# Performance work log

Measured on AMD Instinct MI355X. Metric: run time of the kernel, lower is better.

The kernel has to match this reference:

```python
import jax, jax.numpy as jnp
import numpy as np

N_HEADS = 32
ROPE_THETA = 10000.0


def _rope_cos_sin(sl, head_dim, dtype):
    # inv_freq over even dims, HF/Llama convention: emb = concat(freqs, freqs)
    inv_freq = 1.0 / (ROPE_THETA ** (jnp.arange(0, head_dim, 2, dtype=jnp.float32) / head_dim))
    pos = jnp.arange(sl, dtype=jnp.float32)
    freqs = pos[:, None] * inv_freq[None, :]            # [sl, hd/2]
    emb = jnp.concatenate([freqs, freqs], axis=-1)       # [sl, hd]
    return jnp.cos(emb).astype(dtype), jnp.sin(emb).astype(dtype)


def _rotate_half(x):
    h = x.shape[-1] // 2
    return jnp.concatenate([-x[..., h:], x[..., :h]], axis=-1)


def setup_inputs() -> dict:
    key = jax.random.key(0)
    ks = jax.random.split(key, 5)
    bs, sl, hs = 2, 2048, 4096
    scale = hs ** -0.5
    return {
        "hidden_states": jax.random.normal(ks[0], (bs, sl, hs), jnp.float32),
        "wq": jax.random.normal(ks[1], (hs, hs), jnp.float32) * scale,
        "wk": jax.random.normal(ks[2], (hs, hs), jnp.float32) * scale,
        "wv": jax.random.normal(ks[3], (hs, hs), jnp.float32) * scale,
        "wo": jax.random.normal(ks[4], (hs, hs), jnp.float32) * scale,
    }


def reference(hidden_states, wq, wk, wv, wo):
    bs, sl, hs = hidden_states.shape
    hd = hs // N_HEADS
    # QKV projections (nn.Linear without bias: x @ W.T; here W stored as [in,out])
    q = hidden_states @ wq
    k = hidden_states @ wk
    v = hidden_states @ wv
    # [bs, sl, H, hd]
    q = q.reshape(bs, sl, N_HEADS, hd)
    k = k.reshape(bs, sl, N_HEADS, hd)
    v = v.reshape(bs, sl, N_HEADS, hd)
    # Vectorized RoPE across the whole sequence (original loops per position)
    cos, sin = _rope_cos_sin(sl, hd, hidden_states.dtype)   # [sl, hd]
    cos = cos[None, :, None, :]
    sin = sin[None, :, None, :]
    q = q * cos + _rotate_half(q) * sin
    k = k * cos + _rotate_half(k) * sin
    # causal SDPA, [bs, H, sl, hd]
    q = q.transpose(0, 2, 1, 3)
    k = k.transpose(0, 2, 1, 3)
    v = v.transpose(0, 2, 1, 3)
    scores = jnp.einsum("bhqd,bhkd->bhqk", q, k) / jnp.sqrt(jnp.asarray(hd, q.dtype))
    causal = jnp.tril(jnp.ones((sl, sl), dtype=bool))
    scores = jnp.where(causal[None, None], scores, jnp.finfo(scores.dtype).min)
    attn = jax.nn.softmax(scores, axis=-1)
    out = jnp.einsum("bhqk,bhkd->bhqd", attn, v)
    out = out.transpose(0, 2, 1, 3).reshape(bs, sl, hs)
    return out @ wo
```

## Files before the change

### kernel.cpp

```cpp
#include <hip/hip_runtime.h>
#include <cstdint>
#include <cstddef>

#define SL 2048
#define BS 2
#define NH 32
#define HD 128
#define HS 4096
#define NTOK 4096
#define LDQ 12288

typedef __attribute__((ext_vector_type(8))) short short8;
typedef __attribute__((ext_vector_type(4))) float f32x4;
typedef __attribute__((ext_vector_type(4))) unsigned short u16x4;
typedef __attribute__((ext_vector_type(8))) unsigned short u16x8;

static __device__ __forceinline__ unsigned short f2bf(float f) {
    unsigned int u = __builtin_bit_cast(unsigned int, f);
    u = u + 0x7FFFu + ((u >> 16) & 1u);
    return (unsigned short)(u >> 16);
}
static __device__ __forceinline__ float bf2f(unsigned short h) {
    unsigned int u = ((unsigned int)h) << 16;
    return __builtin_bit_cast(float, u);
}
static __device__ __forceinline__ float fexp2(float x) {
    return __builtin_amdgcn_exp2f(x);
}

static __device__ __forceinline__ f32x4 mfma16(short8 a, short8 b, f32x4 c) {
    return __builtin_amdgcn_mfma_f32_16x16x32_bf16(a, b, c, 0, 0, 0);
}

static __device__ __forceinline__ void gload_lds16(const void* g, void* dst) {
    __builtin_amdgcn_global_load_lds(
        (const __attribute__((address_space(1))) unsigned int*)g,
        (__attribute__((address_space(3))) unsigned int*)dst,
        16, 0, 0);
}

__global__ void k_convert(const float* __restrict__ in, unsigned short* __restrict__ out, int n8) {
    int stride = gridDim.x * blockDim.x;
    for (int i = blockIdx.x * blockDim.x + threadIdx.x; i < n8; i += stride) {
        const f32x4* p = (const f32x4*)in + (size_t)i * 2;
        f32x4 a = p[0], b = p[1];
        u16x8 o;
        o[0] = f2bf(a[0]); o[1] = f2bf(a[1]); o[2] = f2bf(a[2]); o[3] = f2bf(a[3]);
        o[4] = f2bf(b[0]); o[5] = f2bf(b[1]); o[6] = f2bf(b[2]); o[7] = f2bf(b[3]);
        *((u16x8*)out + i) = o;
    }
}

__global__ void k_transpose_w4(const float* __restrict__ w0, const float* __restrict__ w1,
                               const float* __restrict__ w2, const float* __restrict__ w3,
                               unsigned short* __restrict__ wtbase) {
    __shared__ float t[32][33];
    int z = blockIdx.z;
    const float* w = (z == 0) ? w0 : (z == 1) ? w1 : (z == 2) ? w2 : w3;
    unsigned short* wt = wtbase + (size_t)z * HS * HS;
    int r0 = blockIdx.y << 5, c0 = blockIdx.x << 5;
    int tr = threadIdx.x >> 3;
    int tc = (threadIdx.x & 7) << 2;
    f32x4 v = *(const f32x4*)(w + (size_t)(r0 + tr) * HS + c0 + tc);
    t[tr][tc + 0] = v[0]; t[tr][tc + 1] = v[1]; t[tr][tc + 2] = v[2]; t[tr][tc + 3] = v[3];
    __syncthreads();
    u16x4 o;
    o[0] = f2bf(t[tc + 0][tr]); o[1] = f2bf(t[tc + 1][tr]);
    o[2] = f2bf(t[tc + 2][tr]); o[3] = f2bf(t[tc + 3][tr]);
    *(u16x4*)(wt + (size_t)(c0 + tr) * HS + r0 + tc) = o;
}

#define REG(b, w) ((b) * 65536 + (w) * 16384)

template <typename OutT>
__global__ __launch_bounds__(512, 2) void k_gemm256(
    const unsigned short* __restrict__ A,
    const unsigned short* __restrict__ Bt,
    OutT* __restrict__ C,
    int M, int N, int K)
{
    __shared__ char lds[131072];
    char* ldsb = lds;
    int tiles_m = M >> 8, tiles_n = N >> 8;
    int xcd = blockIdx.x & 7, idx = blockIdx.x >> 3;
    int rows_per = tiles_m >> 1, cols_per = tiles_n >> 2;
    int cr = xcd >> 2, cc = xcd & 3;
    int tm = cr * rows_per + idx / cols_per;
    int tn = cc * cols_per + idx % cols_per;
    int tid = threadIdx.x, lane = tid & 63, wave = tid >> 6;
    int l15 = lane & 15, kh = lane >> 4;
    int wm = wave >> 2, wn = wave & 3;
    int row0 = tm << 8, col0 = tn << 8;
    f32x4 acc[8][4] = {};

    int sr = tid >> 3;
    int scb = (tid & 7) << 4;
    int scol = (scb ^ ((sr & 7) << 4)) >> 1;
    const unsigned short* Abase0 = A + (size_t)(row0 + sr) * K + scol;
    const unsigned short* Bbase0 = Bt + (size_t)(col0 + sr) * K + scol;

    int rswz = (l15 & 7) << 4;
    int afb = wm * 16384 + l15 * 128 + ((kh * 16) ^ rswz);
    int bfb = 32768 + ((wn >> 1) * 16384) + (((wn & 1) * 64 + l15) * 128) + ((kh * 16) ^ rswz);

    short8 af[4][2], bfr[4][2];

#define STAGE(R, Gp) do { \
    gload_lds16((Gp),                ldsb + (R) + tid * 16); \
    gload_lds16((Gp) + (size_t)64 * K, ldsb + (R) + 8192 + tid * 16); } while (0)

#define READ_A(buf, g) { _Pragma("unroll") for (int mq = 0; mq < 4; ++mq) \
    _Pragma("unroll") for (int ks = 0; ks < 2; ++ks) \
        af[mq][ks] = *(const short8*)(ldsb + (buf) * 65536 + ((afb + (g) * 8192 + mq * 2048) ^ (ks * 64))); }

#define READ_B2(buf, p) { _Pragma("unroll") for (int n = 2*(p); n < 2*(p)+2; ++n) \
    _Pragma("unroll") for (int ks = 0; ks < 2; ++ks) \
        bfr[n][ks] = *(const short8*)(ldsb + (buf) * 65536 + ((bfb + n * 2048) ^ (ks * 64))); }

#define MFMA_Q(g, nh) { _Pragma("unroll") for (int mq = 0; mq < 4; ++mq) \
    _Pragma("unroll") for (int n2 = 0; n2 < 2; ++n2) { \
        acc[(g)*4+mq][(nh)*2+n2] = mfma16(af[mq][0], bfr[(nh)*2+n2][0], acc[(g)*4+mq][(nh)*2+n2]); \
        acc[(g)*4+mq][(nh)*2+n2] = mfma16(af[mq][1], bfr[(nh)*2+n2][1], acc[(g)*4+mq][(nh)*2+n2]); } }

#define LGKM0() do { asm volatile("s_waitcnt lgkmcnt(0)" ::: "memory"); \
                     __builtin_amdgcn_sched_barrier(0); } while (0)
#define BAR() __builtin_amdgcn_s_barrier()
#define PRIO1() __builtin_amdgcn_s_setprio(1)
#define PRIO0() __builtin_amdgcn_s_setprio(0)
#define VM6() asm volatile("s_waitcnt vmcnt(6)" ::: "memory")
#define VM0() asm volatile("s_waitcnt vmcnt(0)" ::: "memory")

    STAGE(REG(0, 2), Bbase0);
    STAGE(REG(0, 3), Bbase0 + (size_t)128 * K);
    STAGE(REG(0, 0), Abase0);
    STAGE(REG(0, 1), Abase0 + (size_t)128 * K);
    STAGE(REG(1, 2), Bbase0 + 64);
    STAGE(REG(1, 3), Bbase0 + (size_t)128 * K + 64);

    int nkt = K >> 6;
    int niter = nkt >> 1;
    #pragma unroll 1
    for (int t = 0; t < niter; ++t) {
        int kt1 = 2 * t + 1, kt2 = 2 * t + 2, kt3 = 2 * t + 3;
        bool s2 = kt2 < nkt, s3 = kt3 < nkt;
        STAGE(REG(1, 0), Abase0 + (size_t)kt1 * 64);
        VM6();
        BAR();
        READ_B2(0, 0); READ_A(0, 0); LGKM0();
        PRIO1(); MFMA_Q(0, 0); PRIO0();
        READ_B2(0, 1);
        STAGE(REG(1, 1), Abase0 + (size_t)128 * K + (size_t)kt1 * 64);
        BAR(); LGKM0();
        PRIO1(); MFMA_Q(0, 1); PRIO0();
        READ_A(0, 1);
        if (s2) STAGE(REG(0, 2), Bbase0 + (size_t)kt2 * 64);
        BAR(); LGKM0();
        PRIO1(); MFMA_Q(1, 0); PRIO0();
        if (s2) STAGE(REG(0, 3), Bbase0 + (size_t)128 * K + (size_t)kt2 * 64);
        BAR();
        PRIO1(); MFMA_Q(1, 1); PRIO0();
        if (s2) { STAGE(REG(0, 0), Abase0 + (size_t)kt2 * 64); VM6(); }
        else    { VM0(); }
        BAR();
        READ_B2(1, 0); READ_A(1, 0); LGKM0();
        PRIO1(); MFMA_Q(0, 0); PRIO0();
        READ_B2(1, 1);
        if (s2) STAGE(REG(0, 1), Abase0 + (size_t)128 * K + (size_t)kt2 * 64);
        BAR(); LGKM0();
        PRIO1(); MFMA_Q(0, 1); PRIO0();
        READ_A(1, 1);
        if (s3) STAGE(REG(1, 2), Bbase0 + (size_t)kt3 * 64);
        BAR(); LGKM0();
        PRIO1(); MFMA_Q(1, 0); PRIO0();
        if (s3) STAGE(REG(1, 3), Bbase0 + (size_t)128 * K + (size_t)kt3 * 64);
        BAR();
        PRIO1(); MFMA_Q(1, 1); PRIO0();
    }

    #pragma unroll
    for (int m = 0; m < 8; ++m)
        #pragma unroll
        for (int n = 0; n < 4; ++n)
            #pragma unroll
            for (int rr = 0; rr < 4; ++rr) {
                int row = row0 + wm * 128 + m * 16 + kh * 4 + rr;
                int col = col0 + wn * 64 + n * 16 + l15;
                float v = acc[m][n][rr];
                if constexpr (sizeof(OutT) == 2) C[(size_t)row * N + col] = (OutT)f2bf(v);
                else                             C[(size_t)row * N + col] = v;
            }
#undef STAGE
#undef READ_A
#undef READ_B2
#undef MFMA_Q
#undef LGKM0
#undef BAR
#undef PRIO1
#undef PRIO0
#undef VM6
#undef VM0
}

__global__ void k_rope_tv(unsigned short* __restrict__ QKV, unsigned short* __restrict__ Vt) {
    __shared__ unsigned short t[32][36];
    if (blockIdx.x < 8192) {
        const float SCALE = 0.12751779544166854f;
        int i = blockIdx.x * blockDim.x + threadIdx.x;
        int q4 = i & 15;
        int head = (i >> 4) & (NH - 1);
        int tok = i >> 9;
        int s = tok & (SL - 1);
        int d0 = q4 << 2;
        size_t base = (size_t)tok * LDQ + head * HD;
        unsigned short* Q = QKV + base;
        unsigned short* K = QKV + base + HS;
        float cs[4], sn[4];
        #pragma unroll
        for (int j = 0; j < 4; j++) {
            float invf = expf(-(float)(d0 + j) * 0.14391156831212787f);
            float ang = (float)s * invf;
            sn[j] = sinf(ang); cs[j] = cosf(ang);
        }
        {
            u16x4 lo = *(u16x4*)(Q + d0);
            u16x4 hi = *(u16x4*)(Q + d0 + 64);
            u16x4 nlo, nhi;
            #pragma unroll
            for (int j = 0; j < 4; j++) {
                float x0 = bf2f(lo[j]), x1 = bf2f(hi[j]);
                nlo[j] = f2bf((x0 * cs[j] - x1 * sn[j]) * SCALE);
                nhi[j] = f2bf((x1 * cs[j] + x0 * sn[j]) * SCALE);
            }
            *(u16x4*)(Q + d0) = nlo;
            *(u16x4*)(Q + d0 + 64) = nhi;
        }
        {
            u16x4 lo = *(u16x4*)(K + d0);
            u16x4 hi = *(u16x4*)(K + d0 + 64);
            u16x4 nlo, nhi;
            #pragma unroll
            for (int j = 0; j < 4; j++) {
                float x0 = bf2f(lo[j]), x1 = bf2f(hi[j]);
                nlo[j] = f2bf(x0 * cs[j] - x1 * sn[j]);
                nhi[j] = f2bf(x1 * cs[j] + x0 * sn[j]);
            }
            *(u16x4*)(K + d0) = nlo;
            *(u16x4*)(K + d0 + 64) = nhi;
        }
    } else {
        int idx = blockIdx.x - 8192;
        int bh = idx >> 8;
        int b = bh >> 5, h = bh & 31;
        int s0 = (idx & 63) << 5, d0 = ((idx >> 6) & 3) << 5;
        int tr = threadIdx.x >> 3, tc = (threadIdx.x & 7) << 2;
        u16x4 v = *(const u16x4*)(QKV + (size_t)(b * SL + s0 + tr) * LDQ + 2 * HS + h * HD + d0 + tc);
        t[tr][tc + 0] = v[0]; t[tr][tc + 1] = v[1]; t[tr][tc + 2] = v[2]; t[tr][tc + 3] = v[3];
        __syncthreads();
        u16x4 o;
        o[0] = t[tc + 0][tr]; o[1] = t[tc + 1][tr]; o[2] = t[tc + 2][tr]; o[3] = t[tc + 3][tr];
        *(u16x4*)(Vt + ((size_t)(b * NH + h) * HD + d0 + tr) * SL + s0 + tc) = o;
    }
}

__global__ __launch_bounds__(512, 4) void k_attn(
    const unsigned short* __restrict__ QKV,
    const unsigned short* __restrict__ Vt,
    unsigned short* __restrict__ O)
{
    __shared__ unsigned short Ks[64 * 128];
    __shared__ unsigned short Vs[2][128 * 64];
    __shared__ unsigned short Ps[8][16][36];
    int qt = (int)(gridDim.x - 1) - (int)blockIdx.x;
    int bh = blockIdx.y;
    int b = bh >> 5, h = bh & 31;
    int tid = threadIdx.x, lane = tid & 63, wave = tid >> 6;
    int l15 = lane & 15, kh = lane >> 4;
    int qrow0 = (qt << 7) + (wave << 4);
    short8 qf[4];
    {
        const unsigned short* qp = QKV + ((size_t)(b * SL) + qrow0 + l15) * LDQ + h * HD + kh * 8;
        #pragma unroll
        for (int f = 0; f < 4; ++f) qf[f] = *(const short8*)(qp + f * 32);
    }
    f32x4 oacc[8] = {};
    float m[4] = {-1e30f, -1e30f, -1e30f, -1e30f};
    float lsum[4] = {0.f, 0.f, 0.f, 0.f};
    int ksrow = tid >> 4, kchunk = tid & 15;
    int vsrow = tid >> 3, vchunk = tid & 7;
    const unsigned short* Kbase = QKV + HS + (size_t)(b * SL) * LDQ + h * HD;
    const unsigned short* Vbase = Vt + (size_t)(b * NH + h) * HD * (size_t)SL;
    int ktmax = (qt << 1) + 1;

    #pragma unroll
    for (int c = 0; c < 2; ++c) {
        int kr = c * 32 + ksrow;
        gload_lds16(Kbase + (size_t)kr * LDQ + ((kchunk ^ (kr & 7)) << 3),
                    (char*)Ks + c * 8192 + tid * 16);
        int vr = c * 64 + vsrow;
        gload_lds16(Vbase + (size_t)vr * SL + ((vchunk ^ (vr & 7)) << 3),
                    (char*)Vs[0] + c * 8192 + tid * 16);
    }
    int buf = 0;
    for (int kt = 0; kt <= ktmax; ++kt) {
        __syncthreads();
        bool active = (kt << 6) <= qrow0 + 15;
        f32x4 sfr[4];
        if (active) {
            __builtin_amdgcn_s_setprio(1);
            #pragma unroll
            for (int c = 0; c < 4; ++c) {
                f32x4 acc = {};
                int krow = c * 16 + l15;
                #pragma unroll
                for (int f = 0; f < 4; ++f) {
                    short8 kf = *(const short8*)((const char*)Ks + krow * 256 + ((((f << 2) + kh) ^ (krow & 7)) << 4));
                    acc = mfma16(qf[f], kf, acc);
                }
                sfr[c] = acc;
            }
            __builtin_amdgcn_s_setprio(0);
        }
        __syncthreads();
        if (kt < ktmax) {
            #pragma unroll
            for (int c = 0; c < 2; ++c) {
                int kr = c * 32 + ksrow;
                gload_lds16(Kbase + (size_t)(((kt + 1) << 6) + kr) * LDQ + ((kchunk ^ (kr & 7)) << 3),
                            (char*)Ks + c * 8192 + tid * 16);
                int vr = c * 64 + vsrow;
                gload_lds16(Vbase + (size_t)vr * SL + ((kt + 1) << 6) + ((vchunk ^ (vr & 7)) << 3),
                            (char*)Vs[buf ^ 1] + c * 8192 + tid * 16);
            }
        }
        if (active) {
            float pm[4] = {-1e30f, -1e30f, -1e30f, -1e30f};
            bool domask = ((kt << 6) + 63) > qrow0;
            if (domask) {
                #pragma unroll
                for (int c = 0; c < 4; ++c) {
                    int kkg = (kt << 6) + c * 16 + l15;
                    #pragma unroll
                    for (int r = 0; r < 4; ++r) {
                        int qg = qrow0 + kh * 4 + r;
                        float v = sfr[c][r];
                        v = (kkg > qg) ? -1e30f : v;
                        sfr[c][r] = v;
                        pm[r] = fmaxf(pm[r], v);
                    }
                }
            } else {
                #pragma unroll
                for (int c = 0; c < 4; ++c)
                    #pragma unroll
                    for (int r = 0; r < 4; ++r) pm[r] = fmaxf(pm[r], sfr[c][r]);
            }
            #pragma unroll
            for (int off = 1; off < 16; off <<= 1)
                #pragma unroll
                for (int r = 0; r < 4; ++r) pm[r] = fmaxf(pm[r], __shfl_xor(pm[r], off, 64));
            bool ok = true;
            #pragma unroll
            for (int r = 0; r < 4; ++r) ok = ok && (pm[r] <= m[r] + 11.5f);
            if (!__all(ok)) {
                #pragma unroll
                for (int r = 0; r < 4; ++r) {
                    float mn = fmaxf(m[r], pm[r]);
                    float alpha = fexp2(m[r] - mn);
                    m[r] = mn;
                    lsum[r] *= alpha;
                    #pragma unroll
                    for (int db = 0; db < 8; ++db) oacc[db][r] *= alpha;
                }
            }
            float rs[4] = {0.f, 0.f, 0.f, 0.f};
            #pragma unroll
            for (int c = 0; c < 4; ++c)
                #pragma unroll
                for (int r = 0; r < 4; ++r) {
                    float p = fexp2(sfr[c][r] - m[r]);
                    sfr[c][r] = p;
                    rs[r] += p;
                }
            #pragma unroll
            for (int off = 1; off < 16; off <<= 1)
                #pragma unroll
                for (int r = 0; r < 4; ++r) rs[r] += __shfl_xor(rs[r], off, 64);
            #pragma unroll
            for (int r = 0; r < 4; ++r) lsum[r] += rs[r];
            short8 pa[2];
            #pragma unroll
            for (int half = 0; half < 2; ++half) {
                #pragma unroll
                for (int c = 0; c < 2; ++c)
                    #pragma unroll
                    for (int r = 0; r < 4; ++r)
                        Ps[wave][kh * 4 + r][c * 16 + l15] = f2bf(sfr[half * 2 + c][r]);
                pa[half] = *(const short8*)(&Ps[wave][l15][kh * 8]);
            }
            const char* vb = (const char*)Vs[buf];
            __builtin_amdgcn_s_setprio(1);
            #pragma unroll
            for (int db = 0; db < 8; ++db) {
                int vrow = db * 16 + l15;
                #pragma unroll
                for (int f = 0; f < 2; ++f) {
                    short8 vf = *(const short8*)(vb + vrow * 128 + ((((f << 2) + kh) ^ (vrow & 7)) << 4));
                    oacc[db] = mfma16(pa[f], vf, oacc[db]);
                }
            }
            __builtin_amdgcn_s_setprio(0);
        }
        buf ^= 1;
    }
    #pragma unroll
    for (int db = 0; db < 8; ++db)
        #pragma unroll
        for (int r = 0; r < 4; ++r) {
            int qg = qrow0 + kh * 4 + r;
            float v = oacc[db][r] / lsum[r];
            O[((size_t)(b * SL) + qg) * HS + h * HD + db * 16 + l15] = f2bf(v);
        }
}

extern "C" void kernel_launch(void* const* d_in, const int* in_sizes, int n_in,
                              void* d_out, int out_size, void* d_ws, size_t ws_size,
                              hipStream_t stream)
{
    const float* X  = (const float*)d_in[0];
    const float* Wq = (const float*)d_in[1];
    const float* Wk = (const float*)d_in[2];
    const float* Wv = (const float*)d_in[3];
    const float* Wo = (const float*)d_in[4];
    float* out = (float*)d_out;
    const size_t SLAB = (size_t)NTOK * HS * 2;
    char* ws = (char*)d_ws;
    unsigned short* Xb  = (unsigned short*)(ws + 0 * SLAB);
    unsigned short* Wqt = (unsigned short*)(ws + 1 * SLAB);
    unsigned short* Wot = (unsigned short*)(ws + 4 * SLAB);
    unsigned short* QKV = (unsigned short*)(ws + 5 * SLAB);
    unsigned short* Vtb = Xb;
    unsigned short* Ob  = Wqt;

    k_convert<<<2048, 256, 0, stream>>>(X, Xb, NTOK * HS / 8);
    k_transpose_w4<<<dim3(128, 128, 4), 256, 0, stream>>>(Wq, Wk, Wv, Wo, Wqt);
    k_gemm256<unsigned short><<<768, 512, 0, stream>>>(Xb, Wqt, QKV, NTOK, 3 * HS, HS);
    k_rope_tv<<<24576, 256, 0, stream>>>(QKV, Vtb);
    k_attn<<<dim3(SL / 128, BS * NH), 512, 0, stream>>>(QKV, Vtb, Ob);
    k_gemm256<float><<<256, 512, 0, stream>>>(Ob, Wot, out, NTOK, HS, HS);
}
```

Baseline: 813.7 us.

## Double-buffer K tiles in attention and stage GEMM epilogue through LDS

The attention kernel now double-buffers the K tile in shared memory, so the prefetch of the next K/V tile can be issued right after the loop-top barrier instead of after a second mid-iteration barrier. That removes one __syncthreads per key tile and overlaps the loads with the QK^T MFMAs. Separately, the GEMM epilogue writes each wave's accumulators to LDS and reads them back row-contiguous, so global stores become 16-byte vectorized instead of scattered 2- or 4-byte stores. The change costs extra LDS for attention (more shared memory per block, which may reduce occupancy) and an LDS round-trip in the GEMM epilogue, which relies on the GEMM's LDS buffer being free after the added barrier.

```diff
diff --git a/kernel.cpp b/kernel.cpp
--- a/kernel.cpp
+++ b/kernel.cpp
@@ -177,18 +177,33 @@
         PRIO1(); MFMA_Q(1, 1); PRIO0();
     }
 
-    #pragma unroll
-    for (int m = 0; m < 8; ++m)
-        #pragma unroll
-        for (int n = 0; n < 4; ++n)
-            #pragma unroll
-            for (int rr = 0; rr < 4; ++rr) {
-                int row = row0 + wm * 128 + m * 16 + kh * 4 + rr;
-                int col = col0 + wn * 64 + n * 16 + l15;
-                float v = acc[m][n][rr];
-                if constexpr (sizeof(OutT) == 2) C[(size_t)row * N + col] = (OutT)f2bf(v);
-                else                             C[(size_t)row * N + col] = v;
-            }
+    BAR();
+    {
+        float* ep = (float*)(ldsb + wave * 4352);
+        int r16 = lane & 15, cg = lane >> 4;
+        #pragma unroll 1
+        for (int m = 0; m < 8; ++m) {
+            #pragma unroll
+            for (int n = 0; n < 4; ++n)
+                #pragma unroll
+                for (int rr = 0; rr < 4; ++rr)
+                    ep[(kh * 4 + rr) * 68 + n * 16 + l15] = acc[m][n][rr];
+            const float* src = ep + r16 * 68 + cg * 16;
+            int row = row0 + wm * 128 + m * 16 + r16;
+            int col = col0 + wn * 64 + cg * 16;
+            if constexpr (sizeof(OutT) == 2) {
+                u16x8 o0, o1;
+                #pragma unroll
+                for (int i = 0; i < 8; ++i) { o0[i] = f2bf(src[i]); o1[i] = f2bf(src[8 + i]); }
+                *(u16x8*)((unsigned short*)C + (size_t)row * N + col) = o0;
+                *(u16x8*)((unsigned short*)C + (size_t)row * N + col + 8) = o1;
+            } else {
+                #pragma unroll
+                for (int i = 0; i < 4; ++i)
+                    *(f32x4*)((float*)C + (size_t)row * N + col + i * 4) = *(const f32x4*)(src + i * 4);
+            }
+        }
+    }
 #undef STAGE
 #undef READ_A
 #undef READ_B2
@@ -267,7 +282,7 @@
     const unsigned short* __restrict__ Vt,
     unsigned short* __restrict__ O)
 {
-    __shared__ unsigned short Ks[64 * 128];
+    __shared__ unsigned short Ks[2][64 * 128];
     __shared__ unsigned short Vs[2][128 * 64];
     __shared__ unsigned short Ps[8][16][36];
     int qt = (int)(gridDim.x - 1) - (int)blockIdx.x;
@@ -295,7 +310,7 @@
     for (int c = 0; c < 2; ++c) {
         int kr = c * 32 + ksrow;
         gload_lds16(Kbase + (size_t)kr * LDQ + ((kchunk ^ (kr & 7)) << 3),
-                    (char*)Ks + c * 8192 + tid * 16);
+                    (char*)Ks[0] + c * 8192 + tid * 16);
         int vr = c * 64 + vsrow;
         gload_lds16(Vbase + (size_t)vr * SL + ((vchunk ^ (vr & 7)) << 3),
                     (char*)Vs[0] + c * 8192 + tid * 16);
@@ -303,9 +318,20 @@
     int buf = 0;
     for (int kt = 0; kt <= ktmax; ++kt) {
         __syncthreads();
+        if (kt < ktmax) {
+            #pragma unroll
+            for (int c = 0; c < 2; ++c) {
+                int kr = c * 32 + ksrow;
+                gload_lds16(Kbase + (size_t)(((kt + 1) << 6) + kr) * LDQ + ((kchunk ^ (kr & 7)) << 3),
+                            (char*)Ks[buf ^ 1] + c * 8192 + tid * 16);
+                int vr = c * 64 + vsrow;
+                gload_lds16(Vbase + (size_t)vr * SL + ((kt + 1) << 6) + ((vchunk ^ (vr & 7)) << 3),
+                            (char*)Vs[buf ^ 1] + c * 8192 + tid * 16);
+            }
+        }
         bool active = (kt << 6) <= qrow0 + 15;
-        f32x4 sfr[4];
         if (active) {
+            f32x4 sfr[4];
             __builtin_amdgcn_s_setprio(1);
             #pragma unroll
             for (int c = 0; c < 4; ++c) {
@@ -313,26 +339,12 @@
                 int krow = c * 16 + l15;
                 #pragma unroll
                 for (int f = 0; f < 4; ++f) {
-                    short8 kf = *(const short8*)((const char*)Ks + krow * 256 + ((((f << 2) + kh) ^ (krow & 7)) << 4));
+                    short8 kf = *(const short8*)((const char*)Ks[buf] + krow * 256 + ((((f << 2) + kh) ^ (krow & 7)) << 4));
                     acc = mfma16(qf[f], kf, acc);
                 }
                 sfr[c] = acc;
             }
             __builtin_amdgcn_s_setprio(0);
-        }
-        __syncthreads();
-        if (kt < ktmax) {
-            #pragma unroll
-            for (int c = 0; c < 2; ++c) {
-                int kr = c * 32 + ksrow;
-                gload_lds16(Kbase + (size_t)(((kt + 1) << 6) + kr) * LDQ + ((kchunk ^ (kr & 7)) << 3),
-                            (char*)Ks + c * 8192 + tid * 16);
-                int vr = c * 64 + vsrow;
-                gload_lds16(Vbase + (size_t)vr * SL + ((kt + 1) << 6) + ((vchunk ^ (vr & 7)) << 3),
-                            (char*)Vs[buf ^ 1] + c * 8192 + tid * 16);
-            }
-        }
-        if (active) {
             float pm[4] = {-1e30f, -1e30f, -1e30f, -1e30f};
             bool domask = ((kt << 6) + 63) > qrow0;
             if (domask) {
```

Result: slower. 984.0 us (+20.9%).
